# Performance work log

Measured on AMD Instinct MI355X. Metric: run time of the kernel, lower is better.

## Reference

```python
import jax, jax.numpy as jnp
import numpy as np

N, E, H = 50000, 800000, 64
EPS = 1e-5


def _layer_norm(x, gamma, beta):
    mu = jnp.mean(x, axis=-1, keepdims=True)
    var = jnp.mean((x - mu) ** 2, axis=-1, keepdims=True)
    return (x - mu) * jax.lax.rsqrt(var + EPS) * gamma + beta


def setup_inputs() -> dict:
    key = jax.random.key(0)
    ks = jax.random.split(key, 20)
    s = 1.0 / np.sqrt(H)

    def lin(k, din, dout):
        kw, kb = jax.random.split(k)
        return (jax.random.uniform(kw, (din, dout), jnp.float32, -s, s),
                jax.random.uniform(kb, (dout,), jnp.float32, -s, s))

    Ws, bs = lin(ks[0], H, H)            # src_proj
    We, be = lin(ks[1], H, H)            # edge_proj
    Wg, bg = lin(ks[2], 3 * H, H)        # edge_gate
    Wn1, bn1 = lin(ks[3], 2 * H, H)      # node_update[0]
    Wn2, bn2 = lin(ks[4], H, H)          # node_update[2]
    We1, be1 = lin(ks[5], 3 * H, H)      # edge_update[0]
    We2, be2 = lin(ks[6], H, H)          # edge_update[2]

    return {
        'node_feats': jax.random.normal(ks[7], (N, H), jnp.float32),
        'edge_feats': jax.random.normal(ks[8], (E, H), jnp.float32),
        'src': jax.random.randint(ks[9], (E,), 0, N, jnp.int32),
        'dst': jax.random.randint(ks[10], (E,), 0, N, jnp.int32),
        'Ws': Ws, 'bs': bs, 'We': We, 'be': be, 'Wg': Wg, 'bg': bg,
        'Wn1': Wn1, 'bn1': bn1, 'Wn2': Wn2, 'bn2': bn2,
        'We1': We1, 'be1': be1, 'We2': We2, 'be2': be2,
        'g_node': jnp.ones((H,), jnp.float32), 'b_node': jnp.zeros((H,), jnp.float32),
        'g_edge': jnp.ones((H,), jnp.float32), 'b_edge': jnp.zeros((H,), jnp.float32),
    }


def reference(node_feats, edge_feats, src, dst,
              Ws, bs, We, be, Wg, bg,
              Wn1, bn1, Wn2, bn2,
              We1, be1, We2, be2,
              g_node, b_node, g_edge, b_edge):
    h_src = node_feats[src]                      # [E, H]
    h_dst = node_feats[dst]                      # [E, H]
    edge_input = jnp.concatenate([h_src, h_dst, edge_feats], axis=-1)  # [E, 3H]

    gate = jax.nn.sigmoid(edge_input @ Wg + bg)                  # [E, H]
    msg = gate * (h_src @ Ws + bs + edge_feats @ We + be)        # [E, H]
    e_update = jax.nn.silu(edge_input @ We1 + be1) @ We2 + be2   # [E, H]

    agg = jax.ops.segment_sum(msg, dst, num_segments=node_feats.shape[0])  # [N, H]

    node_input = jnp.concatenate([node_feats, agg], axis=-1)     # [N, 2H]
    node_mlp = jax.nn.silu(node_input @ Wn1 + bn1) @ Wn2 + bn2
    node_out = _layer_norm(node_feats + node_mlp, g_node, b_node)
    edge_out = _layer_norm(edge_feats + e_update, g_edge, b_edge)
    return node_out, edge_out
```

## Files before the change

### kernel.cpp

```cpp
#include <hip/hip_runtime.h>


typedef __attribute__((ext_vector_type(8))) short bf16x8;
typedef __attribute__((ext_vector_type(4))) float f32x4;

#define FR_WG   0
#define FR_WE1  1536
#define FR_WS   3072
#define FR_WE   3584
#define FR_WE2  4096
#define FR_WN1  4608
#define FR_WN2  5632
#define FR_TOTAL 6144
#define AGG_OFF_BYTES (FR_TOTAL * 16)

#define EDGE_SMEM 66560
#define NODE_SMEM (128 * 136 * 2)

__device__ __forceinline__ float bf2f(unsigned short u) {
  union { unsigned int i; float f; } v; v.i = ((unsigned int)u) << 16; return v.f;
}
__device__ __forceinline__ unsigned short f2bf(float f) {
  union { float f; unsigned int i; } v; v.f = f;
  unsigned int x = v.i;
  return (unsigned short)((x + 0x7FFFu + ((x >> 16) & 1u)) >> 16);
}
__device__ __forceinline__ float frcp(float x) { return __builtin_amdgcn_rcpf(x); }
__device__ __forceinline__ float sigm(float x) { return frcp(1.0f + __expf(-x)); }

typedef __fp16 fp16x2 __attribute__((ext_vector_type(2)));
__device__ __forceinline__ unsigned int pkf16(float lo, float hi) {
  union { fp16x2 h; unsigned int u; } c;
  c.h = __builtin_amdgcn_cvt_pkrtz(lo, hi);
  return c.u;
}

__device__ __forceinline__ bf16x8 ld8(const void* base, size_t elem, bool f32) {
  if (f32) {
    const float* p = (const float*)base + elem;
    float4 a = *reinterpret_cast<const float4*>(p);
    float4 b = *reinterpret_cast<const float4*>(p + 4);
    bf16x8 r;
    r[0] = (short)f2bf(a.x); r[1] = (short)f2bf(a.y);
    r[2] = (short)f2bf(a.z); r[3] = (short)f2bf(a.w);
    r[4] = (short)f2bf(b.x); r[5] = (short)f2bf(b.y);
    r[6] = (short)f2bf(b.z); r[7] = (short)f2bf(b.w);
    return r;
  }
  return *reinterpret_cast<const bf16x8*>((const unsigned short*)base + elem);
}
__device__ __forceinline__ float ld1(const void* base, size_t i, bool f32) {
  return f32 ? ((const float*)base)[i] : bf2f(((const unsigned short*)base)[i]);
}
__device__ __forceinline__ void st1(void* base, size_t i, float v, bool f32) {
  if (f32) ((float*)base)[i] = v;
  else     ((unsigned short*)base)[i] = f2bf(v);
}
__device__ __forceinline__ unsigned short ldbf(const void* W, size_t i, bool f32) {
  return f32 ? f2bf(((const float*)W)[i]) : ((const unsigned short*)W)[i];
}

extern "C" __global__ void egc_setup(const void* __restrict__ Wg, const void* __restrict__ We1,
                                     const void* __restrict__ Ws, const void* __restrict__ We,
                                     const void* __restrict__ We2, const void* __restrict__ Wn1,
                                     const void* __restrict__ Wn2, const void* __restrict__ gref,
                                     unsigned short* __restrict__ img) {
  const bool f32 = (*(const unsigned int*)gref) == 0x3F800000u;
  int t = blockIdx.x * 256 + threadIdx.x;
  if (t >= FR_TOTAL) return;
  const void* W; int nks, l;
  if (t < FR_WE1)      { W = Wg;  nks = 6; l = t; }
  else if (t < FR_WS)  { W = We1; nks = 6; l = t - FR_WE1; }
  else if (t < FR_WE)  { W = Ws;  nks = 2; l = t - FR_WS; }
  else if (t < FR_WE2) { W = We;  nks = 2; l = t - FR_WE; }
  else if (t < FR_WN1) { W = We2; nks = 2; l = t - FR_WE2; }
  else if (t < FR_WN2) { W = Wn1; nks = 4; l = t - FR_WN1; }
  else                 { W = Wn2; nks = 2; l = t - FR_WN2; }
  int lane = l & 63, fi = l >> 6;
  int ks = fi % nks, ct = fi / nks;
  int col = ct * 16 + (lane & 15);
  int k0 = ks * 32 + (lane >> 4) * 8;
  bf16x8 r;
#pragma unroll
  for (int j = 0; j < 8; ++j)
    r[j] = (short)ldbf(W, (size_t)(k0 + j) * 64 + col, f32);
  *reinterpret_cast<bf16x8*>(img + (size_t)t * 8) = r;
}

extern "C" __global__ void __launch_bounds__(512, 4)
egc_edge(const void* __restrict__ node, const void* __restrict__ ef,
         const int* __restrict__ src, const int* __restrict__ dst,
         const bf16x8* __restrict__ imgf,
         const void* __restrict__ bs, const void* __restrict__ be,
         const void* __restrict__ bg, const void* __restrict__ be1,
         const void* __restrict__ be2,
         const void* __restrict__ g_edge, const void* __restrict__ b_edge,
         unsigned short* __restrict__ aggh, void* __restrict__ out, int E, int N)
{
  extern __shared__ char smem[];
  bf16x8* lwg = (bf16x8*)smem;
  unsigned short* sh = (unsigned short*)(smem + 49152);
  int* dstL = (int*)(smem + 66048);

  const bool f32 = (*(const unsigned int*)g_edge) == 0x3F800000u;
  const int tid = threadIdx.x;
  const int e0 = blockIdx.x * 128;

  {
    const uint4* gs = (const uint4*)imgf;
    uint4* ld = (uint4*)smem;
#pragma unroll
    for (int i = 0; i < 6; ++i) ld[tid + i * 512] = gs[tid + i * 512];
  }
  if (tid < 128) { int ge = e0 + tid; dstL[tid] = dst[ge < E ? ge : E - 1]; }

  const int lane = tid & 63;
  const int wid = tid >> 6;
  const int q = lane & 15, g = lane >> 4;
  const int rowbase = wid * 16;
  const int arow = rowbase + q;

  int ge = e0 + arow; if (ge >= E) ge = E - 1;
  const int se = src[ge], de = dst[ge];
  bf16x8 af[6];
  af[0] = ld8(node, (size_t)se * 64 + g * 8, f32);
  af[1] = ld8(node, (size_t)se * 64 + 32 + g * 8, f32);
  af[2] = ld8(node, (size_t)de * 64 + g * 8, f32);
  af[3] = ld8(node, (size_t)de * 64 + 32 + g * 8, f32);
  af[4] = ld8(ef, (size_t)ge * 64 + g * 8, f32);
  af[5] = ld8(ef, (size_t)ge * 64 + 32 + g * 8, f32);
  *reinterpret_cast<bf16x8*>(sh + arow * 66 + g * 8) = af[4];
  *reinterpret_cast<bf16x8*>(sh + arow * 66 + 32 + g * 8) = af[5];

  __syncthreads();

  const f32x4 zero = {0.f, 0.f, 0.f, 0.f};
  f32x4 accG[4], accH[4], accM[4];
#pragma unroll
  for (int ct = 0; ct < 4; ++ct) { accG[ct] = zero; accH[ct] = zero; accM[ct] = zero; }

#pragma unroll
  for (int ct = 0; ct < 4; ++ct) {
#pragma unroll
    for (int ks = 0; ks < 6; ++ks) {
      bf16x8 bG = lwg[(ct * 6 + ks) * 64 + lane];
      accG[ct] = __builtin_amdgcn_mfma_f32_16x16x32_bf16(af[ks], bG, accG[ct], 0, 0, 0);
      bf16x8 bH = lwg[FR_WE1 + (ct * 6 + ks) * 64 + lane];
      accH[ct] = __builtin_amdgcn_mfma_f32_16x16x32_bf16(af[ks], bH, accH[ct], 0, 0, 0);
    }
    bf16x8 bm0 = imgf[FR_WS + (ct * 2 + 0) * 64 + lane];
    accM[ct] = __builtin_amdgcn_mfma_f32_16x16x32_bf16(af[0], bm0, accM[ct], 0, 0, 0);
    bf16x8 bm1 = imgf[FR_WS + (ct * 2 + 1) * 64 + lane];
    accM[ct] = __builtin_amdgcn_mfma_f32_16x16x32_bf16(af[1], bm1, accM[ct], 0, 0, 0);
    bf16x8 bm2 = imgf[FR_WE + (ct * 2 + 0) * 64 + lane];
    accM[ct] = __builtin_amdgcn_mfma_f32_16x16x32_bf16(af[4], bm2, accM[ct], 0, 0, 0);
    bf16x8 bm3 = imgf[FR_WE + (ct * 2 + 1) * 64 + lane];
    accM[ct] = __builtin_amdgcn_mfma_f32_16x16x32_bf16(af[5], bm3, accM[ct], 0, 0, 0);
  }

  int rows[4]; int dn[4]; bool vr[4];
#pragma unroll
  for (int r = 0; r < 4; ++r) {
    rows[r] = rowbase + g * 4 + r;
    vr[r] = (e0 + rows[r]) < E;
    dn[r] = dstL[rows[r]];
  }

  float efr[4][4];
#pragma unroll
  for (int ct = 0; ct < 4; ++ct)
#pragma unroll
    for (int r = 0; r < 4; ++r)
      efr[ct][r] = bf2f(sh[rows[r] * 66 + ct * 16 + q]);

  const bool odd = (q & 1);
#pragma unroll
  for (int ct = 0; ct < 4; ++ct) {
    const int col = ct * 16 + q;
    const float bgv = ld1(bg, col, f32);
    const float bmv = ld1(bs, col, f32) + ld1(be, col, f32);
    const float b1v = ld1(be1, col, f32);
    float mv[4];
#pragma unroll
    for (int r = 0; r < 4; ++r) {
      float gv = sigm(accG[ct][r] + bgv);
      mv[r] = gv * (accM[ct][r] + bmv);
      float hv = accH[ct][r] + b1v;
      sh[rows[r] * 66 + col] = f2bf(hv * sigm(hv));
    }
#pragma unroll
    for (int rp = 0; rp < 2; ++rp) {
      float a0 = mv[2 * rp], a1 = mv[2 * rp + 1];
      float b0 = __shfl_xor(a0, 1), b1 = __shfl_xor(a1, 1);
      float lo = odd ? b1 : a0;
      float hi = odd ? a1 : b0;
      int rr = 2 * rp + (odd ? 1 : 0);
      if (vr[rr]) {
        unsigned int data = pkf16(lo, hi);
        unsigned long long addr = (unsigned long long)(aggh + (size_t)dn[rr] * 64 + ct * 16 + (q & ~1));
        asm volatile("global_atomic_pk_add_f16 %0, %1, off" :: "v"(addr), "v"(data) : "memory");
      }
    }
  }

  bf16x8 au0 = *reinterpret_cast<const bf16x8*>(sh + arow * 66 + g * 8);
  bf16x8 au1 = *reinterpret_cast<const bf16x8*>(sh + arow * 66 + 32 + g * 8);
  f32x4 accU[4];
#pragma unroll
  for (int ct = 0; ct < 4; ++ct) {
    bf16x8 b0 = imgf[FR_WE2 + (ct * 2 + 0) * 64 + lane];
    accU[ct] = __builtin_amdgcn_mfma_f32_16x16x32_bf16(au0, b0, zero, 0, 0, 0);
    bf16x8 b1 = imgf[FR_WE2 + (ct * 2 + 1) * 64 + lane];
    accU[ct] = __builtin_amdgcn_mfma_f32_16x16x32_bf16(au1, b1, accU[ct], 0, 0, 0);
  }

  f32x4 x[4];
#pragma unroll
  for (int ct = 0; ct < 4; ++ct) {
    const int col = ct * 16 + q;
    const float b2v = ld1(be2, col, f32);
#pragma unroll
    for (int r = 0; r < 4; ++r)
      x[ct][r] = efr[ct][r] + accU[ct][r] + b2v;
  }
  f32x4 s = x[0] + x[1] + x[2] + x[3];
  f32x4 s2 = x[0] * x[0] + x[1] * x[1] + x[2] * x[2] + x[3] * x[3];
#pragma unroll
  for (int m = 1; m < 16; m <<= 1) {
    s[0] += __shfl_xor(s[0], m); s[1] += __shfl_xor(s[1], m);
    s[2] += __shfl_xor(s[2], m); s[3] += __shfl_xor(s[3], m);
    s2[0] += __shfl_xor(s2[0], m); s2[1] += __shfl_xor(s2[1], m);
    s2[2] += __shfl_xor(s2[2], m); s2[3] += __shfl_xor(s2[3], m);
  }
  f32x4 mu, inv;
#pragma unroll
  for (int r = 0; r < 4; ++r) {
    float m = s[r] * 0.015625f;
    mu[r] = m;
    inv[r] = rsqrtf(s2[r] * 0.015625f - m * m + 1e-5f);
  }

#pragma unroll
  for (int ct = 0; ct < 4; ++ct) {
    const int col = ct * 16 + q;
    const float gv = ld1(g_edge, col, f32);
    const float bv = ld1(b_edge, col, f32);
#pragma unroll
    for (int r = 0; r < 4; ++r) {
      if (vr[r])
        st1(out, (size_t)(N + e0 + rows[r]) * 64 + col,
            (x[ct][r] - mu[r]) * inv[r] * gv + bv, f32);
    }
  }
}

extern "C" __global__ void __launch_bounds__(512, 8)
egc_node(const void* __restrict__ node, const unsigned short* __restrict__ aggh,
         const bf16x8* __restrict__ imgf,
         const void* __restrict__ bn1, const void* __restrict__ bn2,
         const void* __restrict__ g_node, const void* __restrict__ b_node,
         void* __restrict__ out, int N)
{
  extern __shared__ char smem[];
  unsigned short* ni = (unsigned short*)smem;

  const bool f32 = (*(const unsigned int*)g_node) == 0x3F800000u;
  const int tid = threadIdx.x;
  const int r0 = blockIdx.x * 128;

  for (int i = tid; i < 128 * 16; i += 512) {
    int e = i >> 4, c = i & 15;
    int gr = r0 + e; if (gr >= N) gr = N - 1;
    if (c < 8) {
      *reinterpret_cast<bf16x8*>(ni + e * 136 + c * 8) =
          ld8(node, (size_t)gr * 64 + c * 8, f32);
    } else {
      int c2 = c - 8;
      uint4 v = *reinterpret_cast<const uint4*>(aggh + (size_t)gr * 64 + c2 * 8);
      const __fp16* hp = reinterpret_cast<const __fp16*>(&v);
      bf16x8 t;
#pragma unroll
      for (int j = 0; j < 8; ++j) t[j] = (short)f2bf((float)hp[j]);
      *reinterpret_cast<bf16x8*>(ni + e * 136 + 64 + c2 * 8) = t;
    }
  }
  __syncthreads();

  const int lane = tid & 63;
  const int wid = tid >> 6;
  const int q = lane & 15, g = lane >> 4;
  const int rowbase = wid * 16;

  bf16x8 af[4];
#pragma unroll
  for (int ks = 0; ks < 4; ++ks)
    af[ks] = *reinterpret_cast<const bf16x8*>(ni + (rowbase + q) * 136 + ks * 32 + g * 8);

  const f32x4 zero = {0.f, 0.f, 0.f, 0.f};
  f32x4 acc1[4];
#pragma unroll
  for (int ct = 0; ct < 4; ++ct) acc1[ct] = zero;
#pragma unroll
  for (int ct = 0; ct < 4; ++ct) {
#pragma unroll
    for (int ks = 0; ks < 4; ++ks) {
      bf16x8 b = imgf[FR_WN1 + (ct * 4 + ks) * 64 + lane];
      acc1[ct] = __builtin_amdgcn_mfma_f32_16x16x32_bf16(af[ks], b, acc1[ct], 0, 0, 0);
    }
  }

  int rows[4]; bool vr[4];
#pragma unroll
  for (int r = 0; r < 4; ++r) {
    rows[r] = rowbase + g * 4 + r;
    vr[r] = (r0 + rows[r]) < N;
  }

#pragma unroll
  for (int ct = 0; ct < 4; ++ct) {
    const int col = ct * 16 + q;
    const float b1v = ld1(bn1, col, f32);
#pragma unroll
    for (int r = 0; r < 4; ++r) {
      float hv = acc1[ct][r] + b1v;
      ni[rows[r] * 136 + 64 + col] = f2bf(hv * sigm(hv));
    }
  }

  bf16x8 au0 = *reinterpret_cast<const bf16x8*>(ni + (rowbase + q) * 136 + 64 + g * 8);
  bf16x8 au1 = *reinterpret_cast<const bf16x8*>(ni + (rowbase + q) * 136 + 96 + g * 8);
  f32x4 acc2[4];
#pragma unroll
  for (int ct = 0; ct < 4; ++ct) {
    bf16x8 b0 = imgf[FR_WN2 + (ct * 2 + 0) * 64 + lane];
    acc2[ct] = __builtin_amdgcn_mfma_f32_16x16x32_bf16(au0, b0, zero, 0, 0, 0);
    bf16x8 b1 = imgf[FR_WN2 + (ct * 2 + 1) * 64 + lane];
    acc2[ct] = __builtin_amdgcn_mfma_f32_16x16x32_bf16(au1, b1, acc2[ct], 0, 0, 0);
  }

  f32x4 x[4];
#pragma unroll
  for (int ct = 0; ct < 4; ++ct) {
    const int col = ct * 16 + q;
    const float b2v = ld1(bn2, col, f32);
#pragma unroll
    for (int r = 0; r < 4; ++r)
      x[ct][r] = bf2f(ni[rows[r] * 136 + col]) + acc2[ct][r] + b2v;
  }
  f32x4 s = x[0] + x[1] + x[2] + x[3];
  f32x4 s2 = x[0] * x[0] + x[1] * x[1] + x[2] * x[2] + x[3] * x[3];
#pragma unroll
  for (int m = 1; m < 16; m <<= 1) {
    s[0] += __shfl_xor(s[0], m); s[1] += __shfl_xor(s[1], m);
    s[2] += __shfl_xor(s[2], m); s[3] += __shfl_xor(s[3], m);
    s2[0] += __shfl_xor(s2[0], m); s2[1] += __shfl_xor(s2[1], m);
    s2[2] += __shfl_xor(s2[2], m); s2[3] += __shfl_xor(s2[3], m);
  }
  f32x4 mu, inv;
#pragma unroll
  for (int r = 0; r < 4; ++r) {
    float m = s[r] * 0.015625f;
    mu[r] = m;
    inv[r] = rsqrtf(s2[r] * 0.015625f - m * m + 1e-5f);
  }

#pragma unroll
  for (int ct = 0; ct < 4; ++ct) {
    const int col = ct * 16 + q;
    const float gv = ld1(g_node, col, f32);
    const float bv = ld1(b_node, col, f32);
#pragma unroll
    for (int r = 0; r < 4; ++r) {
      if (vr[r])
        st1(out, (size_t)(r0 + rows[r]) * 64 + col,
            (x[ct][r] - mu[r]) * inv[r] * gv + bv, f32);
    }
  }
}

extern "C" void kernel_launch(void* const* d_in, const int* in_sizes, int n_in,
                              void* d_out, int out_size, void* d_ws, size_t ws_size,
                              hipStream_t stream)
{
  const void* node = d_in[0];
  const void* ef   = d_in[1];
  const int* src = (const int*)d_in[2];
  const int* dst = (const int*)d_in[3];
  const void* Ws  = d_in[4];  const void* bs  = d_in[5];
  const void* We  = d_in[6];  const void* be  = d_in[7];
  const void* Wg  = d_in[8];  const void* bg  = d_in[9];
  const void* Wn1 = d_in[10]; const void* bn1 = d_in[11];
  const void* Wn2 = d_in[12]; const void* bn2 = d_in[13];
  const void* We1 = d_in[14]; const void* be1 = d_in[15];
  const void* We2 = d_in[16]; const void* be2 = d_in[17];
  const void* g_node = d_in[18]; const void* b_node = d_in[19];
  const void* g_edge = d_in[20]; const void* b_edge = d_in[21];

  const int N = in_sizes[0] / 64;
  const int E = in_sizes[2];

  unsigned short* img = (unsigned short*)d_ws;
  unsigned short* aggh = (unsigned short*)((char*)d_ws + AGG_OFF_BYTES);
  hipMemsetAsync(aggh, 0, (size_t)N * 64 * sizeof(unsigned short), stream);

  egc_setup<<<(FR_TOTAL + 255) / 256, 256, 0, stream>>>(Wg, We1, Ws, We, We2, Wn1, Wn2,
                                                        g_edge, img);

  hipFuncSetAttribute((const void*)egc_edge, hipFuncAttributeMaxDynamicSharedMemorySize,
                      EDGE_SMEM);

  const int eblocks = (E + 127) / 128;
  egc_edge<<<eblocks, 512, EDGE_SMEM, stream>>>(node, ef, src, dst,
      (const bf16x8*)img, bs, be, bg, be1, be2, g_edge, b_edge, aggh, d_out, E, N);

  const int nblocks = (N + 127) / 128;
  egc_node<<<nblocks, 512, NODE_SMEM, stream>>>(node, aggh, (const bf16x8*)img,
      bn1, bn2, g_node, b_node, d_out, N);
}
```

Measured before the change: 313.9 us.

## Make edge kernel persistent with software-prefetched gathers for next tile

Converts the edge kernel to a persistent grid of up to 512 blocks that loop over 128-edge tiles. Weights are loaded into LDS once per block instead of once per tile. The gather for the next tile is issued while the current tile's epilogue runs, so gather latency overlaps compute. Other changes: dst indices are loaded as int4 instead of through LDS, the MFMA accumulators are split into two column groups to reduce register pressure, and the edge-feature residual is folded into the MFMA accumulator init. The costs are more live registers from the prefetch buffers and fewer blocks in flight, which may leave latency exposed. The atomic asm also drops its memory clobber.

```diff
diff --git a/kernel.cpp b/kernel.cpp
--- a/kernel.cpp
+++ b/kernel.cpp
@@ -14,7 +14,7 @@
 #define FR_TOTAL 6144
 #define AGG_OFF_BYTES (FR_TOTAL * 16)
 
-#define EDGE_SMEM 66560
+#define EDGE_SMEM 66048
 #define NODE_SMEM (128 * 136 * 2)
 
 __device__ __forceinline__ float bf2f(unsigned short u) {
@@ -58,6 +58,15 @@
 }
 __device__ __forceinline__ unsigned short ldbf(const void* W, size_t i, bool f32) {
   return f32 ? f2bf(((const float*)W)[i]) : ((const unsigned short*)W)[i];
+}
+__device__ __forceinline__ int4 load_dn(const int* __restrict__ dst, int base, int E) {
+  if (base + 3 < E) return *reinterpret_cast<const int4*>(dst + base);
+  int4 v;
+  v.x = dst[base < E ? base : E - 1];
+  v.y = dst[base + 1 < E ? base + 1 : E - 1];
+  v.z = dst[base + 2 < E ? base + 2 : E - 1];
+  v.w = dst[base + 3 < E ? base + 3 : E - 1];
+  return v;
 }
 
 extern "C" __global__ void egc_setup(const void* __restrict__ Wg, const void* __restrict__ We1,
@@ -87,6 +96,14 @@
   *reinterpret_cast<bf16x8*>(img + (size_t)t * 8) = r;
 }
 
+#define GATHER(afv, se_, de_, ge_)                            \
+  afv[0] = ld8(node, (size_t)(se_) * 64 + g * 8, f32);        \
+  afv[1] = ld8(node, (size_t)(se_) * 64 + 32 + g * 8, f32);   \
+  afv[2] = ld8(node, (size_t)(de_) * 64 + g * 8, f32);        \
+  afv[3] = ld8(node, (size_t)(de_) * 64 + 32 + g * 8, f32);   \
+  afv[4] = ld8(ef, (size_t)(ge_) * 64 + g * 8, f32);          \
+  afv[5] = ld8(ef, (size_t)(ge_) * 64 + 32 + g * 8, f32);
+
 extern "C" __global__ void __launch_bounds__(512, 4)
 egc_edge(const void* __restrict__ node, const void* __restrict__ ef,
          const int* __restrict__ src, const int* __restrict__ dst,
@@ -100,11 +117,9 @@
   extern __shared__ char smem[];
   bf16x8* lwg = (bf16x8*)smem;
   unsigned short* sh = (unsigned short*)(smem + 49152);
-  int* dstL = (int*)(smem + 66048);
 
   const bool f32 = (*(const unsigned int*)g_edge) == 0x3F800000u;
   const int tid = threadIdx.x;
-  const int e0 = blockIdx.x * 128;
 
   {
     const uint4* gs = (const uint4*)imgf;
@@ -112,145 +127,164 @@
 #pragma unroll
     for (int i = 0; i < 6; ++i) ld[tid + i * 512] = gs[tid + i * 512];
   }
-  if (tid < 128) { int ge = e0 + tid; dstL[tid] = dst[ge < E ? ge : E - 1]; }
 
   const int lane = tid & 63;
   const int wid = tid >> 6;
   const int q = lane & 15, g = lane >> 4;
   const int rowbase = wid * 16;
   const int arow = rowbase + q;
-
-  int ge = e0 + arow; if (ge >= E) ge = E - 1;
-  const int se = src[ge], de = dst[ge];
-  bf16x8 af[6];
-  af[0] = ld8(node, (size_t)se * 64 + g * 8, f32);
-  af[1] = ld8(node, (size_t)se * 64 + 32 + g * 8, f32);
-  af[2] = ld8(node, (size_t)de * 64 + g * 8, f32);
-  af[3] = ld8(node, (size_t)de * 64 + 32 + g * 8, f32);
-  af[4] = ld8(ef, (size_t)ge * 64 + g * 8, f32);
-  af[5] = ld8(ef, (size_t)ge * 64 + 32 + g * 8, f32);
-  *reinterpret_cast<bf16x8*>(sh + arow * 66 + g * 8) = af[4];
-  *reinterpret_cast<bf16x8*>(sh + arow * 66 + 32 + g * 8) = af[5];
+  const bool odd = (q & 1);
+  const int nt = (E + 127) >> 7;
+  const int stride = gridDim.x;
+  const f32x4 zero = {0.f, 0.f, 0.f, 0.f};
 
   __syncthreads();
 
-  const f32x4 zero = {0.f, 0.f, 0.f, 0.f};
-  f32x4 accG[4], accH[4], accM[4];
-#pragma unroll
-  for (int ct = 0; ct < 4; ++ct) { accG[ct] = zero; accH[ct] = zero; accM[ct] = zero; }
-
-#pragma unroll
-  for (int ct = 0; ct < 4; ++ct) {
-#pragma unroll
-    for (int ks = 0; ks < 6; ++ks) {
-      bf16x8 bG = lwg[(ct * 6 + ks) * 64 + lane];
-      accG[ct] = __builtin_amdgcn_mfma_f32_16x16x32_bf16(af[ks], bG, accG[ct], 0, 0, 0);
-      bf16x8 bH = lwg[FR_WE1 + (ct * 6 + ks) * 64 + lane];
-      accH[ct] = __builtin_amdgcn_mfma_f32_16x16x32_bf16(af[ks], bH, accH[ct], 0, 0, 0);
-    }
-    bf16x8 bm0 = imgf[FR_WS + (ct * 2 + 0) * 64 + lane];
-    accM[ct] = __builtin_amdgcn_mfma_f32_16x16x32_bf16(af[0], bm0, accM[ct], 0, 0, 0);
-    bf16x8 bm1 = imgf[FR_WS + (ct * 2 + 1) * 64 + lane];
-    accM[ct] = __builtin_amdgcn_mfma_f32_16x16x32_bf16(af[1], bm1, accM[ct], 0, 0, 0);
-    bf16x8 bm2 = imgf[FR_WE + (ct * 2 + 0) * 64 + lane];
-    accM[ct] = __builtin_amdgcn_mfma_f32_16x16x32_bf16(af[4], bm2, accM[ct], 0, 0, 0);
-    bf16x8 bm3 = imgf[FR_WE + (ct * 2 + 1) * 64 + lane];
-    accM[ct] = __builtin_amdgcn_mfma_f32_16x16x32_bf16(af[5], bm3, accM[ct], 0, 0, 0);
-  }
-
-  int rows[4]; int dn[4]; bool vr[4];
-#pragma unroll
-  for (int r = 0; r < 4; ++r) {
-    rows[r] = rowbase + g * 4 + r;
-    vr[r] = (e0 + rows[r]) < E;
-    dn[r] = dstL[rows[r]];
-  }
-
-  float efr[4][4];
-#pragma unroll
-  for (int ct = 0; ct < 4; ++ct)
-#pragma unroll
-    for (int r = 0; r < 4; ++r)
-      efr[ct][r] = bf2f(sh[rows[r] * 66 + ct * 16 + q]);
-
-  const bool odd = (q & 1);
-#pragma unroll
-  for (int ct = 0; ct < 4; ++ct) {
-    const int col = ct * 16 + q;
-    const float bgv = ld1(bg, col, f32);
-    const float bmv = ld1(bs, col, f32) + ld1(be, col, f32);
-    const float b1v = ld1(be1, col, f32);
-    float mv[4];
+  int t = blockIdx.x;
+  int ge = t * 128 + arow; if (ge >= E) ge = E - 1;
+  int se = src[ge], de = dst[ge];
+  bf16x8 af[6], afn[6];
+  GATHER(af, se, de, ge);
+  int4 dnv = load_dn(dst, t * 128 + rowbase + g * 4, E);
+
+  for (;;) {
+    const int e0 = t * 128;
+    const int tn = t + stride;
+    const bool more = (tn < nt);
+
+    int ge_n = 0, se_n = 0, de_n = 0; int4 dn_n = make_int4(0, 0, 0, 0);
+    if (more) {
+      ge_n = tn * 128 + arow; if (ge_n >= E) ge_n = E - 1;
+      se_n = src[ge_n]; de_n = dst[ge_n];
+      dn_n = load_dn(dst, tn * 128 + rowbase + g * 4, E);
+    }
+
+    int rows[4]; bool vr[4]; int dn[4];
+    dn[0] = dnv.x; dn[1] = dnv.y; dn[2] = dnv.z; dn[3] = dnv.w;
 #pragma unroll
     for (int r = 0; r < 4; ++r) {
-      float gv = sigm(accG[ct][r] + bgv);
-      mv[r] = gv * (accM[ct][r] + bmv);
-      float hv = accH[ct][r] + b1v;
-      sh[rows[r] * 66 + col] = f2bf(hv * sigm(hv));
-    }
-#pragma unroll
-    for (int rp = 0; rp < 2; ++rp) {
-      float a0 = mv[2 * rp], a1 = mv[2 * rp + 1];
-      float b0 = __shfl_xor(a0, 1), b1 = __shfl_xor(a1, 1);
-      float lo = odd ? b1 : a0;
-      float hi = odd ? a1 : b0;
-      int rr = 2 * rp + (odd ? 1 : 0);
-      if (vr[rr]) {
-        unsigned int data = pkf16(lo, hi);
-        unsigned long long addr = (unsigned long long)(aggh + (size_t)dn[rr] * 64 + ct * 16 + (q & ~1));
-        asm volatile("global_atomic_pk_add_f16 %0, %1, off" :: "v"(addr), "v"(data) : "memory");
+      rows[r] = rowbase + g * 4 + r;
+      vr[r] = (e0 + rows[r]) < E;
+    }
+
+    *reinterpret_cast<bf16x8*>(sh + arow * 66 + g * 8) = af[4];
+    *reinterpret_cast<bf16x8*>(sh + arow * 66 + 32 + g * 8) = af[5];
+    float efr[4][4];
+#pragma unroll
+    for (int ct = 0; ct < 4; ++ct)
+#pragma unroll
+      for (int r = 0; r < 4; ++r)
+        efr[ct][r] = bf2f(sh[rows[r] * 66 + ct * 16 + q]);
+
+#pragma unroll
+    for (int ctg = 0; ctg < 2; ++ctg) {
+      f32x4 aG[2], aH[2], aM[2];
+#pragma unroll
+      for (int c2 = 0; c2 < 2; ++c2) { aG[c2] = zero; aH[c2] = zero; aM[c2] = zero; }
+#pragma unroll
+      for (int c2 = 0; c2 < 2; ++c2) {
+        const int ct = ctg * 2 + c2;
+#pragma unroll
+        for (int ks = 0; ks < 6; ++ks) {
+          bf16x8 bG = lwg[(ct * 6 + ks) * 64 + lane];
+          aG[c2] = __builtin_amdgcn_mfma_f32_16x16x32_bf16(af[ks], bG, aG[c2], 0, 0, 0);
+          bf16x8 bH = lwg[FR_WE1 + (ct * 6 + ks) * 64 + lane];
+          aH[c2] = __builtin_amdgcn_mfma_f32_16x16x32_bf16(af[ks], bH, aH[c2], 0, 0, 0);
+        }
+        bf16x8 bm0 = imgf[FR_WS + (ct * 2 + 0) * 64 + lane];
+        aM[c2] = __builtin_amdgcn_mfma_f32_16x16x32_bf16(af[0], bm0, aM[c2], 0, 0, 0);
+        bf16x8 bm1 = imgf[FR_WS + (ct * 2 + 1) * 64 + lane];
+        aM[c2] = __builtin_amdgcn_mfma_f32_16x16x32_bf16(af[1], bm1, aM[c2], 0, 0, 0);
+        bf16x8 bm2 = imgf[FR_WE + (ct * 2 + 0) * 64 + lane];
+        aM[c2] = __builtin_amdgcn_mfma_f32_16x16x32_bf16(af[4], bm2, aM[c2], 0, 0, 0);
+        bf16x8 bm3 = imgf[FR_WE + (ct * 2 + 1) * 64 + lane];
+        aM[c2] = __builtin_amdgcn_mfma_f32_16x16x32_bf16(af[5], bm3, aM[c2], 0, 0, 0);
       }
-    }
-  }
-
-  bf16x8 au0 = *reinterpret_cast<const bf16x8*>(sh + arow * 66 + g * 8);
-  bf16x8 au1 = *reinterpret_cast<const bf16x8*>(sh + arow * 66 + 32 + g * 8);
-  f32x4 accU[4];
-#pragma unroll
-  for (int ct = 0; ct < 4; ++ct) {
-    bf16x8 b0 = imgf[FR_WE2 + (ct * 2 + 0) * 64 + lane];
-    accU[ct] = __builtin_amdgcn_mfma_f32_16x16x32_bf16(au0, b0, zero, 0, 0, 0);
-    bf16x8 b1 = imgf[FR_WE2 + (ct * 2 + 1) * 64 + lane];
-    accU[ct] = __builtin_amdgcn_mfma_f32_16x16x32_bf16(au1, b1, accU[ct], 0, 0, 0);
-  }
-
-  f32x4 x[4];
-#pragma unroll
-  for (int ct = 0; ct < 4; ++ct) {
-    const int col = ct * 16 + q;
-    const float b2v = ld1(be2, col, f32);
-#pragma unroll
-    for (int r = 0; r < 4; ++r)
-      x[ct][r] = efr[ct][r] + accU[ct][r] + b2v;
-  }
-  f32x4 s = x[0] + x[1] + x[2] + x[3];
-  f32x4 s2 = x[0] * x[0] + x[1] * x[1] + x[2] * x[2] + x[3] * x[3];
-#pragma unroll
-  for (int m = 1; m < 16; m <<= 1) {
-    s[0] += __shfl_xor(s[0], m); s[1] += __shfl_xor(s[1], m);
-    s[2] += __shfl_xor(s[2], m); s[3] += __shfl_xor(s[3], m);
-    s2[0] += __shfl_xor(s2[0], m); s2[1] += __shfl_xor(s2[1], m);
-    s2[2] += __shfl_xor(s2[2], m); s2[3] += __shfl_xor(s2[3], m);
-  }
-  f32x4 mu, inv;
-#pragma unroll
-  for (int r = 0; r < 4; ++r) {
-    float m = s[r] * 0.015625f;
-    mu[r] = m;
-    inv[r] = rsqrtf(s2[r] * 0.015625f - m * m + 1e-5f);
-  }
-
-#pragma unroll
-  for (int ct = 0; ct < 4; ++ct) {
-    const int col = ct * 16 + q;
-    const float gv = ld1(g_edge, col, f32);
-    const float bv = ld1(b_edge, col, f32);
+#pragma unroll
+      for (int c2 = 0; c2 < 2; ++c2) {
+        const int ct = ctg * 2 + c2;
+        const int col = ct * 16 + q;
+        const float bgv = ld1(bg, col, f32);
+        const float bmv = ld1(bs, col, f32) + ld1(be, col, f32);
+        const float b1v = ld1(be1, col, f32);
+        float mv[4];
+#pragma unroll
+        for (int r = 0; r < 4; ++r) {
+          float gv = sigm(aG[c2][r] + bgv);
+          mv[r] = gv * (aM[c2][r] + bmv);
+          float hv = aH[c2][r] + b1v;
+          sh[rows[r] * 66 + col] = f2bf(hv * sigm(hv));
+        }
+#pragma unroll
+        for (int rp = 0; rp < 2; ++rp) {
+          float a0 = mv[2 * rp], a1 = mv[2 * rp + 1];
+          float b0 = __shfl_xor(a0, 1), b1 = __shfl_xor(a1, 1);
+          float lo = odd ? b1 : a0;
+          float hi = odd ? a1 : b0;
+          int rr = 2 * rp + (odd ? 1 : 0);
+          if (vr[rr]) {
+            unsigned int data = pkf16(lo, hi);
+            unsigned long long addr =
+                (unsigned long long)(aggh + (size_t)dn[rr] * 64 + ct * 16 + (q & ~1));
+            asm volatile("global_atomic_pk_add_f16 %0, %1, off" :: "v"(addr), "v"(data));
+          }
+        }
+      }
+    }
+
+    if (more) { GATHER(afn, se_n, de_n, ge_n); }
+
+    bf16x8 au0 = *reinterpret_cast<const bf16x8*>(sh + arow * 66 + g * 8);
+    bf16x8 au1 = *reinterpret_cast<const bf16x8*>(sh + arow * 66 + 32 + g * 8);
+    f32x4 x[4];
+#pragma unroll
+    for (int ct = 0; ct < 4; ++ct) {
+      f32x4 c0 = {efr[ct][0], efr[ct][1], efr[ct][2], efr[ct][3]};
+      bf16x8 b0 = imgf[FR_WE2 + (ct * 2 + 0) * 64 + lane];
+      x[ct] = __builtin_amdgcn_mfma_f32_16x16x32_bf16(au0, b0, c0, 0, 0, 0);
+      bf16x8 b1 = imgf[FR_WE2 + (ct * 2 + 1) * 64 + lane];
+      x[ct] = __builtin_amdgcn_mfma_f32_16x16x32_bf16(au1, b1, x[ct], 0, 0, 0);
+    }
+#pragma unroll
+    for (int ct = 0; ct < 4; ++ct) {
+      const float b2v = ld1(be2, ct * 16 + q, f32);
+#pragma unroll
+      for (int r = 0; r < 4; ++r) x[ct][r] += b2v;
+    }
+
+    f32x4 s = x[0] + x[1] + x[2] + x[3];
+    f32x4 s2 = x[0] * x[0] + x[1] * x[1] + x[2] * x[2] + x[3] * x[3];
+#pragma unroll
+    for (int m = 1; m < 16; m <<= 1) {
+      s[0] += __shfl_xor(s[0], m); s[1] += __shfl_xor(s[1], m);
+      s[2] += __shfl_xor(s[2], m); s[3] += __shfl_xor(s[3], m);
+      s2[0] += __shfl_xor(s2[0], m); s2[1] += __shfl_xor(s2[1], m);
+      s2[2] += __shfl_xor(s2[2], m); s2[3] += __shfl_xor(s2[3], m);
+    }
+    f32x4 mu, inv;
 #pragma unroll
     for (int r = 0; r < 4; ++r) {
-      if (vr[r])
-        st1(out, (size_t)(N + e0 + rows[r]) * 64 + col,
-            (x[ct][r] - mu[r]) * inv[r] * gv + bv, f32);
-    }
+      float m = s[r] * 0.015625f;
+      mu[r] = m;
+      inv[r] = rsqrtf(s2[r] * 0.015625f - m * m + 1e-5f);
+    }
+#pragma unroll
+    for (int ct = 0; ct < 4; ++ct) {
+      const int col = ct * 16 + q;
+      const float gv = ld1(g_edge, col, f32);
+      const float bv = ld1(b_edge, col, f32);
+#pragma unroll
+      for (int r = 0; r < 4; ++r) {
+        if (vr[r])
+          st1(out, (size_t)(N + e0 + rows[r]) * 64 + col,
+              (x[ct][r] - mu[r]) * inv[r] * gv + bv, f32);
+      }
+    }
+
+    if (!more) break;
+    t = tn; se = se_n; de = de_n; ge = ge_n; dnv = dn_n;
+#pragma unroll
+    for (int j = 0; j < 6; ++j) af[j] = afn[j];
   }
 }
 
@@ -409,7 +443,8 @@
   hipFuncSetAttribute((const void*)egc_edge, hipFuncAttributeMaxDynamicSharedMemorySize,
                       EDGE_SMEM);
 
-  const int eblocks = (E + 127) / 128;
+  const int nt = (E + 127) / 128;
+  const int eblocks = nt < 512 ? nt : 512;
   egc_edge<<<eblocks, 512, EDGE_SMEM, stream>>>(node, ef, src, dst,
       (const bf16x8*)img, bs, be, bg, be1, be2, g_edge, b_edge, aggh, d_out, E, N);
 
```

New measurement: 525.1 us. 1.67x slower.

## Precompute per-node projections and gather them instead of per-edge node GEMMs

Applied to the files above, without the earlier changes.

Adds a per-node pre-pass that multiplies node features by the src/dst slices of Wg and We1 and by Ws once per node (N rows instead of E), storing fp16 results in a table. The edge kernel then gathers these partial products by src/dst and only runs the edge-feature GEMM slices, which cuts MFMA work and removes the LDS weight staging. Edge-feature residual is folded into the We2 MFMA accumulator, and dst indices are loaded as int4. Costs are an extra kernel, wider per-edge gathers (640 B per endpoint vs 128 B of node features), and fp16 rounding of the partial sums.

```diff
diff --git a/kernel.cpp b/kernel.cpp
--- a/kernel.cpp
+++ b/kernel.cpp
@@ -3,6 +3,8 @@
 
 typedef __attribute__((ext_vector_type(8))) short bf16x8;
 typedef __attribute__((ext_vector_type(4))) float f32x4;
+typedef __fp16 fp16x8 __attribute__((ext_vector_type(8)));
+typedef __fp16 fp16x2 __attribute__((ext_vector_type(2)));
 
 #define FR_WG   0
 #define FR_WE1  1536
@@ -13,8 +15,9 @@
 #define FR_WN2  5632
 #define FR_TOTAL 6144
 #define AGG_OFF_BYTES (FR_TOTAL * 16)
-
-#define EDGE_SMEM 66560
+#define PTAB_OFF_SHORTS(N) (AGG_OFF_BYTES / 2 + (size_t)(N) * 64)
+
+#define EDGE_SMEM 68096
 #define NODE_SMEM (128 * 136 * 2)
 
 __device__ __forceinline__ float bf2f(unsigned short u) {
@@ -25,10 +28,14 @@
   unsigned int x = v.i;
   return (unsigned short)((x + 0x7FFFu + ((x >> 16) & 1u)) >> 16);
 }
+__device__ __forceinline__ unsigned short f2h(float x) {
+  union { __fp16 h; unsigned short u; } c; c.h = (__fp16)x; return c.u;
+}
+__device__ __forceinline__ float h2f(unsigned short u) {
+  union { unsigned short u; __fp16 h; } c; c.u = u; return (float)c.h;
+}
 __device__ __forceinline__ float frcp(float x) { return __builtin_amdgcn_rcpf(x); }
 __device__ __forceinline__ float sigm(float x) { return frcp(1.0f + __expf(-x)); }
-
-typedef __fp16 fp16x2 __attribute__((ext_vector_type(2)));
 __device__ __forceinline__ unsigned int pkf16(float lo, float hi) {
   union { fp16x2 h; unsigned int u; } c;
   c.h = __builtin_amdgcn_cvt_pkrtz(lo, hi);
@@ -58,6 +65,15 @@
 }
 __device__ __forceinline__ unsigned short ldbf(const void* W, size_t i, bool f32) {
   return f32 ? f2bf(((const float*)W)[i]) : ((const unsigned short*)W)[i];
+}
+__device__ __forceinline__ int4 load_dn(const int* __restrict__ dst, int base, int E) {
+  if (base + 3 < E) return *reinterpret_cast<const int4*>(dst + base);
+  int4 v;
+  v.x = dst[base < E ? base : E - 1];
+  v.y = dst[base + 1 < E ? base + 1 : E - 1];
+  v.z = dst[base + 2 < E ? base + 2 : E - 1];
+  v.w = dst[base + 3 < E ? base + 3 : E - 1];
+  return v;
 }
 
 extern "C" __global__ void egc_setup(const void* __restrict__ Wg, const void* __restrict__ We1,
@@ -87,10 +103,56 @@
   *reinterpret_cast<bf16x8*>(img + (size_t)t * 8) = r;
 }
 
-extern "C" __global__ void __launch_bounds__(512, 4)
-egc_edge(const void* __restrict__ node, const void* __restrict__ ef,
+extern "C" __global__ void __launch_bounds__(512)
+egc_pre(const void* __restrict__ node, const bf16x8* __restrict__ imgf,
+        const void* __restrict__ gref, unsigned short* __restrict__ ptab, int N)
+{
+  const bool f32 = (*(const unsigned int*)gref) == 0x3F800000u;
+  const int tid = threadIdx.x;
+  const int lane = tid & 63;
+  const int wid = tid >> 6;
+  const int q = lane & 15, g = lane >> 4;
+  const int rowbase = wid * 16;
+  const int r0 = blockIdx.x * 128;
+
+  int gr = r0 + rowbase + q; if (gr >= N) gr = N - 1;
+  bf16x8 a0 = ld8(node, (size_t)gr * 64 + g * 8, f32);
+  bf16x8 a1 = ld8(node, (size_t)gr * 64 + 32 + g * 8, f32);
+
+  const f32x4 zero = {0.f, 0.f, 0.f, 0.f};
+#pragma unroll
+  for (int ct = 0; ct < 4; ++ct) {
+    f32x4 c1 = zero, c2 = zero, c3 = zero, c4 = zero, c5 = zero;
+    c1 = __builtin_amdgcn_mfma_f32_16x16x32_bf16(a0, imgf[FR_WG + (ct * 6 + 0) * 64 + lane], c1, 0, 0, 0);
+    c1 = __builtin_amdgcn_mfma_f32_16x16x32_bf16(a1, imgf[FR_WG + (ct * 6 + 1) * 64 + lane], c1, 0, 0, 0);
+    c2 = __builtin_amdgcn_mfma_f32_16x16x32_bf16(a0, imgf[FR_WG + (ct * 6 + 2) * 64 + lane], c2, 0, 0, 0);
+    c2 = __builtin_amdgcn_mfma_f32_16x16x32_bf16(a1, imgf[FR_WG + (ct * 6 + 3) * 64 + lane], c2, 0, 0, 0);
+    c3 = __builtin_amdgcn_mfma_f32_16x16x32_bf16(a0, imgf[FR_WS + (ct * 2 + 0) * 64 + lane], c3, 0, 0, 0);
+    c3 = __builtin_amdgcn_mfma_f32_16x16x32_bf16(a1, imgf[FR_WS + (ct * 2 + 1) * 64 + lane], c3, 0, 0, 0);
+    c4 = __builtin_amdgcn_mfma_f32_16x16x32_bf16(a0, imgf[FR_WE1 + (ct * 6 + 0) * 64 + lane], c4, 0, 0, 0);
+    c4 = __builtin_amdgcn_mfma_f32_16x16x32_bf16(a1, imgf[FR_WE1 + (ct * 6 + 1) * 64 + lane], c4, 0, 0, 0);
+    c5 = __builtin_amdgcn_mfma_f32_16x16x32_bf16(a0, imgf[FR_WE1 + (ct * 6 + 2) * 64 + lane], c5, 0, 0, 0);
+    c5 = __builtin_amdgcn_mfma_f32_16x16x32_bf16(a1, imgf[FR_WE1 + (ct * 6 + 3) * 64 + lane], c5, 0, 0, 0);
+    const int col = ct * 16 + q;
+#pragma unroll
+    for (int r = 0; r < 4; ++r) {
+      int rowN = r0 + rowbase + g * 4 + r;
+      if (rowN < N) {
+        unsigned short* p = ptab + (size_t)rowN * 320 + col;
+        p[0]   = f2h(c1[r]);
+        p[64]  = f2h(c2[r]);
+        p[128] = f2h(c3[r]);
+        p[192] = f2h(c4[r]);
+        p[256] = f2h(c5[r]);
+      }
+    }
+  }
+}
+
+extern "C" __global__ void __launch_bounds__(512)
+egc_edge(const void* __restrict__ ef,
          const int* __restrict__ src, const int* __restrict__ dst,
-         const bf16x8* __restrict__ imgf,
+         const bf16x8* __restrict__ imgf, const unsigned short* __restrict__ ptab,
          const void* __restrict__ bs, const void* __restrict__ be,
          const void* __restrict__ bg, const void* __restrict__ be1,
          const void* __restrict__ be2,
@@ -98,72 +160,52 @@
          unsigned short* __restrict__ aggh, void* __restrict__ out, int E, int N)
 {
   extern __shared__ char smem[];
-  bf16x8* lwg = (bf16x8*)smem;
-  unsigned short* sh = (unsigned short*)(smem + 49152);
-  int* dstL = (int*)(smem + 66048);
+  unsigned short* pn = (unsigned short*)smem;
+  unsigned short* sh = (unsigned short*)(smem + 51200);
 
   const bool f32 = (*(const unsigned int*)g_edge) == 0x3F800000u;
   const int tid = threadIdx.x;
-  const int e0 = blockIdx.x * 128;
-
-  {
-    const uint4* gs = (const uint4*)imgf;
-    uint4* ld = (uint4*)smem;
-#pragma unroll
-    for (int i = 0; i < 6; ++i) ld[tid + i * 512] = gs[tid + i * 512];
-  }
-  if (tid < 128) { int ge = e0 + tid; dstL[tid] = dst[ge < E ? ge : E - 1]; }
-
   const int lane = tid & 63;
   const int wid = tid >> 6;
   const int q = lane & 15, g = lane >> 4;
   const int rowbase = wid * 16;
   const int arow = rowbase + q;
+  const bool odd = (q & 1);
+  const int e0 = blockIdx.x * 128;
 
   int ge = e0 + arow; if (ge >= E) ge = E - 1;
   const int se = src[ge], de = dst[ge];
-  bf16x8 af[6];
-  af[0] = ld8(node, (size_t)se * 64 + g * 8, f32);
-  af[1] = ld8(node, (size_t)se * 64 + 32 + g * 8, f32);
-  af[2] = ld8(node, (size_t)de * 64 + g * 8, f32);
-  af[3] = ld8(node, (size_t)de * 64 + 32 + g * 8, f32);
-  af[4] = ld8(ef, (size_t)ge * 64 + g * 8, f32);
-  af[5] = ld8(ef, (size_t)ge * 64 + 32 + g * 8, f32);
-  *reinterpret_cast<bf16x8*>(sh + arow * 66 + g * 8) = af[4];
-  *reinterpret_cast<bf16x8*>(sh + arow * 66 + 32 + g * 8) = af[5];
-
-  __syncthreads();
-
-  const f32x4 zero = {0.f, 0.f, 0.f, 0.f};
-  f32x4 accG[4], accH[4], accM[4];
-#pragma unroll
-  for (int ct = 0; ct < 4; ++ct) { accG[ct] = zero; accH[ct] = zero; accM[ct] = zero; }
-
-#pragma unroll
-  for (int ct = 0; ct < 4; ++ct) {
-#pragma unroll
-    for (int ks = 0; ks < 6; ++ks) {
-      bf16x8 bG = lwg[(ct * 6 + ks) * 64 + lane];
-      accG[ct] = __builtin_amdgcn_mfma_f32_16x16x32_bf16(af[ks], bG, accG[ct], 0, 0, 0);
-      bf16x8 bH = lwg[FR_WE1 + (ct * 6 + ks) * 64 + lane];
-      accH[ct] = __builtin_amdgcn_mfma_f32_16x16x32_bf16(af[ks], bH, accH[ct], 0, 0, 0);
-    }
-    bf16x8 bm0 = imgf[FR_WS + (ct * 2 + 0) * 64 + lane];
-    accM[ct] = __builtin_amdgcn_mfma_f32_16x16x32_bf16(af[0], bm0, accM[ct], 0, 0, 0);
-    bf16x8 bm1 = imgf[FR_WS + (ct * 2 + 1) * 64 + lane];
-    accM[ct] = __builtin_amdgcn_mfma_f32_16x16x32_bf16(af[1], bm1, accM[ct], 0, 0, 0);
-    bf16x8 bm2 = imgf[FR_WE + (ct * 2 + 0) * 64 + lane];
-    accM[ct] = __builtin_amdgcn_mfma_f32_16x16x32_bf16(af[4], bm2, accM[ct], 0, 0, 0);
-    bf16x8 bm3 = imgf[FR_WE + (ct * 2 + 1) * 64 + lane];
-    accM[ct] = __builtin_amdgcn_mfma_f32_16x16x32_bf16(af[5], bm3, accM[ct], 0, 0, 0);
-  }
-
-  int rows[4]; int dn[4]; bool vr[4];
+  bf16x8 a0 = ld8(ef, (size_t)ge * 64 + g * 8, f32);
+  bf16x8 a1 = ld8(ef, (size_t)ge * 64 + 32 + g * 8, f32);
+  const unsigned short* Ps = ptab + (size_t)se * 320;
+  const unsigned short* Pd = ptab + (size_t)de * 320;
+  fp16x8 p1a = *reinterpret_cast<const fp16x8*>(Ps + 0 + g * 8);
+  fp16x8 p1b = *reinterpret_cast<const fp16x8*>(Ps + 0 + 32 + g * 8);
+  fp16x8 p2a = *reinterpret_cast<const fp16x8*>(Pd + 64 + g * 8);
+  fp16x8 p2b = *reinterpret_cast<const fp16x8*>(Pd + 64 + 32 + g * 8);
+  fp16x8 p3a = *reinterpret_cast<const fp16x8*>(Ps + 128 + g * 8);
+  fp16x8 p3b = *reinterpret_cast<const fp16x8*>(Ps + 128 + 32 + g * 8);
+  fp16x8 p4a = *reinterpret_cast<const fp16x8*>(Ps + 192 + g * 8);
+  fp16x8 p4b = *reinterpret_cast<const fp16x8*>(Ps + 192 + 32 + g * 8);
+  fp16x8 p5a = *reinterpret_cast<const fp16x8*>(Pd + 256 + g * 8);
+  fp16x8 p5b = *reinterpret_cast<const fp16x8*>(Pd + 256 + 32 + g * 8);
+  int4 dnv = load_dn(dst, e0 + rowbase + g * 4, E);
+
+  *reinterpret_cast<bf16x8*>(sh + arow * 66 + g * 8) = a0;
+  *reinterpret_cast<bf16x8*>(sh + arow * 66 + 32 + g * 8) = a1;
+  *reinterpret_cast<fp16x8*>(pn + arow * 200 + g * 8) = p1a + p2a;
+  *reinterpret_cast<fp16x8*>(pn + arow * 200 + 32 + g * 8) = p1b + p2b;
+  *reinterpret_cast<fp16x8*>(pn + arow * 200 + 64 + g * 8) = p3a;
+  *reinterpret_cast<fp16x8*>(pn + arow * 200 + 64 + 32 + g * 8) = p3b;
+  *reinterpret_cast<fp16x8*>(pn + arow * 200 + 128 + g * 8) = p4a + p5a;
+  *reinterpret_cast<fp16x8*>(pn + arow * 200 + 128 + 32 + g * 8) = p4b + p5b;
+
+  int rows[4]; bool vr[4]; int dn[4];
+  dn[0] = dnv.x; dn[1] = dnv.y; dn[2] = dnv.z; dn[3] = dnv.w;
 #pragma unroll
   for (int r = 0; r < 4; ++r) {
     rows[r] = rowbase + g * 4 + r;
     vr[r] = (e0 + rows[r]) < E;
-    dn[r] = dstL[rows[r]];
   }
 
   float efr[4][4];
@@ -173,7 +215,19 @@
     for (int r = 0; r < 4; ++r)
       efr[ct][r] = bf2f(sh[rows[r] * 66 + ct * 16 + q]);
 
-  const bool odd = (q & 1);
+  const f32x4 zero = {0.f, 0.f, 0.f, 0.f};
+
+  f32x4 aG[4], aH[4], aM[4];
+#pragma unroll
+  for (int ct = 0; ct < 4; ++ct) {
+    aG[ct] = __builtin_amdgcn_mfma_f32_16x16x32_bf16(a0, imgf[FR_WG + (ct * 6 + 4) * 64 + lane], zero, 0, 0, 0);
+    aG[ct] = __builtin_amdgcn_mfma_f32_16x16x32_bf16(a1, imgf[FR_WG + (ct * 6 + 5) * 64 + lane], aG[ct], 0, 0, 0);
+    aH[ct] = __builtin_amdgcn_mfma_f32_16x16x32_bf16(a0, imgf[FR_WE1 + (ct * 6 + 4) * 64 + lane], zero, 0, 0, 0);
+    aH[ct] = __builtin_amdgcn_mfma_f32_16x16x32_bf16(a1, imgf[FR_WE1 + (ct * 6 + 5) * 64 + lane], aH[ct], 0, 0, 0);
+    aM[ct] = __builtin_amdgcn_mfma_f32_16x16x32_bf16(a0, imgf[FR_WE + (ct * 2 + 0) * 64 + lane], zero, 0, 0, 0);
+    aM[ct] = __builtin_amdgcn_mfma_f32_16x16x32_bf16(a1, imgf[FR_WE + (ct * 2 + 1) * 64 + lane], aM[ct], 0, 0, 0);
+  }
+
 #pragma unroll
   for (int ct = 0; ct < 4; ++ct) {
     const int col = ct * 16 + q;
@@ -183,46 +237,44 @@
     float mv[4];
 #pragma unroll
     for (int r = 0; r < 4; ++r) {
-      float gv = sigm(accG[ct][r] + bgv);
-      mv[r] = gv * (accM[ct][r] + bmv);
-      float hv = accH[ct][r] + b1v;
+      const int rb = rows[r] * 200 + col;
+      float gate = sigm(aG[ct][r] + h2f(pn[rb]) + bgv);
+      mv[r] = gate * (aM[ct][r] + h2f(pn[rb + 64]) + bmv);
+      float hv = aH[ct][r] + h2f(pn[rb + 128]) + b1v;
       sh[rows[r] * 66 + col] = f2bf(hv * sigm(hv));
     }
 #pragma unroll
     for (int rp = 0; rp < 2; ++rp) {
-      float a0 = mv[2 * rp], a1 = mv[2 * rp + 1];
-      float b0 = __shfl_xor(a0, 1), b1 = __shfl_xor(a1, 1);
-      float lo = odd ? b1 : a0;
-      float hi = odd ? a1 : b0;
+      float x0 = mv[2 * rp], x1 = mv[2 * rp + 1];
+      float y0 = __shfl_xor(x0, 1), y1 = __shfl_xor(x1, 1);
+      float lo = odd ? y1 : x0;
+      float hi = odd ? x1 : y0;
       int rr = 2 * rp + (odd ? 1 : 0);
       if (vr[rr]) {
         unsigned int data = pkf16(lo, hi);
-        unsigned long long addr = (unsigned long long)(aggh + (size_t)dn[rr] * 64 + ct * 16 + (q & ~1));
-        asm volatile("global_atomic_pk_add_f16 %0, %1, off" :: "v"(addr), "v"(data) : "memory");
+        unsigned long long addr =
+            (unsigned long long)(aggh + (size_t)dn[rr] * 64 + ct * 16 + (q & ~1));
+        asm volatile("global_atomic_pk_add_f16 %0, %1, off" :: "v"(addr), "v"(data));
       }
     }
   }
 
   bf16x8 au0 = *reinterpret_cast<const bf16x8*>(sh + arow * 66 + g * 8);
   bf16x8 au1 = *reinterpret_cast<const bf16x8*>(sh + arow * 66 + 32 + g * 8);
-  f32x4 accU[4];
-#pragma unroll
-  for (int ct = 0; ct < 4; ++ct) {
-    bf16x8 b0 = imgf[FR_WE2 + (ct * 2 + 0) * 64 + lane];
-    accU[ct] = __builtin_amdgcn_mfma_f32_16x16x32_bf16(au0, b0, zero, 0, 0, 0);
-    bf16x8 b1 = imgf[FR_WE2 + (ct * 2 + 1) * 64 + lane];
-    accU[ct] = __builtin_amdgcn_mfma_f32_16x16x32_bf16(au1, b1, accU[ct], 0, 0, 0);
-  }
-
   f32x4 x[4];
 #pragma unroll
   for (int ct = 0; ct < 4; ++ct) {
-    const int col = ct * 16 + q;
-    const float b2v = ld1(be2, col, f32);
-#pragma unroll
-    for (int r = 0; r < 4; ++r)
-      x[ct][r] = efr[ct][r] + accU[ct][r] + b2v;
-  }
+    f32x4 c0 = {efr[ct][0], efr[ct][1], efr[ct][2], efr[ct][3]};
+    x[ct] = __builtin_amdgcn_mfma_f32_16x16x32_bf16(au0, imgf[FR_WE2 + (ct * 2 + 0) * 64 + lane], c0, 0, 0, 0);
+    x[ct] = __builtin_amdgcn_mfma_f32_16x16x32_bf16(au1, imgf[FR_WE2 + (ct * 2 + 1) * 64 + lane], x[ct], 0, 0, 0);
+  }
+#pragma unroll
+  for (int ct = 0; ct < 4; ++ct) {
+    const float b2v = ld1(be2, ct * 16 + q, f32);
+#pragma unroll
+    for (int r = 0; r < 4; ++r) x[ct][r] += b2v;
+  }
+
   f32x4 s = x[0] + x[1] + x[2] + x[3];
   f32x4 s2 = x[0] * x[0] + x[1] * x[1] + x[2] * x[2] + x[3] * x[3];
 #pragma unroll
@@ -239,7 +291,6 @@
     mu[r] = m;
     inv[r] = rsqrtf(s2[r] * 0.015625f - m * m + 1e-5f);
   }
-
 #pragma unroll
   for (int ct = 0; ct < 4; ++ct) {
     const int col = ct * 16 + q;
@@ -332,10 +383,8 @@
   f32x4 acc2[4];
 #pragma unroll
   for (int ct = 0; ct < 4; ++ct) {
-    bf16x8 b0 = imgf[FR_WN2 + (ct * 2 + 0) * 64 + lane];
-    acc2[ct] = __builtin_amdgcn_mfma_f32_16x16x32_bf16(au0, b0, zero, 0, 0, 0);
-    bf16x8 b1 = imgf[FR_WN2 + (ct * 2 + 1) * 64 + lane];
-    acc2[ct] = __builtin_amdgcn_mfma_f32_16x16x32_bf16(au1, b1, acc2[ct], 0, 0, 0);
+    acc2[ct] = __builtin_amdgcn_mfma_f32_16x16x32_bf16(au0, imgf[FR_WN2 + (ct * 2 + 0) * 64 + lane], zero, 0, 0, 0);
+    acc2[ct] = __builtin_amdgcn_mfma_f32_16x16x32_bf16(au1, imgf[FR_WN2 + (ct * 2 + 1) * 64 + lane], acc2[ct], 0, 0, 0);
   }
 
   f32x4 x[4];
@@ -401,17 +450,21 @@
 
   unsigned short* img = (unsigned short*)d_ws;
   unsigned short* aggh = (unsigned short*)((char*)d_ws + AGG_OFF_BYTES);
+  unsigned short* ptab = (unsigned short*)d_ws + PTAB_OFF_SHORTS(N);
   hipMemsetAsync(aggh, 0, (size_t)N * 64 * sizeof(unsigned short), stream);
 
   egc_setup<<<(FR_TOTAL + 255) / 256, 256, 0, stream>>>(Wg, We1, Ws, We, We2, Wn1, Wn2,
                                                         g_edge, img);
 
+  const int pblocks = (N + 127) / 128;
+  egc_pre<<<pblocks, 512, 0, stream>>>(node, (const bf16x8*)img, g_node, ptab, N);
+
   hipFuncSetAttribute((const void*)egc_edge, hipFuncAttributeMaxDynamicSharedMemorySize,
                       EDGE_SMEM);
 
   const int eblocks = (E + 127) / 128;
-  egc_edge<<<eblocks, 512, EDGE_SMEM, stream>>>(node, ef, src, dst,
-      (const bf16x8*)img, bs, be, bg, be1, be2, g_edge, b_edge, aggh, d_out, E, N);
+  egc_edge<<<eblocks, 512, EDGE_SMEM, stream>>>(ef, src, dst, (const bf16x8*)img, ptab,
+      bs, be, bg, be1, be2, g_edge, b_edge, aggh, d_out, E, N);
 
   const int nblocks = (N + 127) / 128;
   egc_node<<<nblocks, 512, NODE_SMEM, stream>>>(node, aggh, (const bf16x8*)img,
```

Result: slower. 391.8 us (+24.8%).
